# Optimization experiments

Hardware: AMD Instinct MI355X
Metric: run time of the kernel (lower is better)

The kernel has to match this reference:

```python
import jax, jax.numpy as jnp
import numpy as np

REG1 = 0.05
REG2 = 0.05

N, D, P = 262144, 256, 512


def setup_inputs() -> dict:
    key = jax.random.key(0)
    kz, kp = jax.random.split(key)
    z = jax.random.normal(kz, (N, D), dtype=jnp.float32)
    # nn.Parameter(torch.rand(P, D)) -> uniform [0, 1)
    prototype_vectors = jax.random.uniform(kp, (P, D), dtype=jnp.float32)
    return {"z": z, "prototype_vectors": prototype_vectors}


def _cdist(a, b):
    # Euclidean pairwise distances [Na, Nb] via the norm trick (matches torch.cdist p=2).
    a2 = jnp.sum(a * a, axis=-1, keepdims=True)          # [Na, 1]
    b2 = jnp.sum(b * b, axis=-1)[None, :]                # [1, Nb]
    sq = a2 + b2 - 2.0 * (a @ b.T)
    return jnp.sqrt(jnp.maximum(sq, 0.0))


def reference(z, prototype_vectors):
    p_dist = _cdist(z, prototype_vectors)                # [N, P]
    f_dist = _cdist(prototype_vectors, z)                # [P, N]
    return (REG1 * jnp.mean(jnp.min(p_dist, axis=1))
            + REG2 * jnp.mean(jnp.min(f_dist, axis=1)))
```

## Files before the change

kernel.cpp:

```cpp
#include <hip/hip_runtime.h>
#include <hip/hip_bf16.h>

#define N_ROWS 262144
#define DDIM   256
#define PROTO  512
#define BM     64
#define RTG    4096
#define NBLK   8192

typedef __bf16 bf16x8 __attribute__((ext_vector_type(8)));
typedef float  f32x4  __attribute__((ext_vector_type(4)));

__global__ void prep_proto(const float* __restrict__ Pm,
                           unsigned short* __restrict__ PBf,
                           float* __restrict__ P2) {
  int p = blockIdx.x;
  int k = threadIdx.x;
  float v = Pm[p * DDIM + k];
  int idx = (p >> 4) * 4096 + (k >> 5) * 512 + ((((k >> 3) & 3) * 16) + (p & 15)) * 8 + (k & 7);
  ((__bf16*)PBf)[idx] = (__bf16)v;
  float sq = v * v;
  #pragma unroll
  for (int m = 1; m < 64; m <<= 1) sq += __shfl_xor(sq, m);
  __shared__ float ws4[4];
  if ((k & 63) == 0) ws4[k >> 6] = sq;
  __syncthreads();
  if (k == 0) P2[p] = (ws4[0] + ws4[1]) + (ws4[2] + ws4[3]);
}

__global__ __launch_bounds__(256, 4)
void proto_main(const float* __restrict__ Z, const unsigned short* __restrict__ PBf,
                const float* __restrict__ P2, float* __restrict__ colpart,
                float* __restrict__ rowminpart) {
  __shared__ __align__(16) unsigned short A_lds[BM * 256];
  __shared__ float z2s[BM];
  __shared__ float rowred[BM * 4];

  const int t   = threadIdx.x;
  const int w   = t >> 6;
  const int l   = t & 63;
  const int l15 = l & 15;
  const int lg  = l >> 4;

  const int bid = blockIdx.x;
  const int g   = ((bid >> 4) << 3) | (bid & 7);
  const int cc  = (bid >> 3) & 1;
  const size_t row0 = (size_t)g * BM;

  const int srow = t >> 2;
  const int sc4  = t & 3;
  {
    const float4* Zv = (const float4*)Z + (row0 + srow) * (DDIM / 4);
    float zacc = 0.f;
    #pragma unroll
    for (int m = 0; m < 8; ++m) {
      float4 a0 = Zv[(sc4 + m * 4) * 2];
      float4 a1 = Zv[(sc4 + m * 4) * 2 + 1];
      zacc += a0.x*a0.x + a0.y*a0.y + a0.z*a0.z + a0.w*a0.w
            + a1.x*a1.x + a1.y*a1.y + a1.z*a1.z + a1.w*a1.w;
      bf16x8 pk;
      pk[0] = (__bf16)a0.x; pk[1] = (__bf16)a0.y; pk[2] = (__bf16)a0.z; pk[3] = (__bf16)a0.w;
      pk[4] = (__bf16)a1.x; pk[5] = (__bf16)a1.y; pk[6] = (__bf16)a1.z; pk[7] = (__bf16)a1.w;
      int slot = (sc4 + m * 4) ^ (srow & 7);
      *(bf16x8*)&A_lds[srow * 256 + slot * 8] = pk;
    }
    zacc += __shfl_xor(zacc, 1);
    zacc += __shfl_xor(zacc, 2);
    if (sc4 == 0) z2s[srow] = zacc;
  }

  float p2r[4];
  #pragma unroll
  for (int j = 0; j < 4; ++j) p2r[j] = P2[cc * 256 + w * 64 + j * 16 + l15];

  __syncthreads();

  f32x4 acc[4][4];
  #pragma unroll
  for (int i = 0; i < 4; ++i)
    #pragma unroll
    for (int j = 0; j < 4; ++j)
      acc[i][j] = (f32x4){0.f, 0.f, 0.f, 0.f};

  const unsigned short* PBw = PBf + (size_t)(cc * 16 + w * 4) * 4096 + l * 8;
  bf16x8 bgn[4];
  #pragma unroll
  for (int j = 0; j < 4; ++j)
    bgn[j] = *(const bf16x8*)&PBw[(size_t)(j * 8) * 512];
  #pragma unroll
  for (int ks = 0; ks < 8; ++ks) {
    bf16x8 bgc[4];
    #pragma unroll
    for (int j = 0; j < 4; ++j) bgc[j] = bgn[j];
    if (ks < 7) {
      #pragma unroll
      for (int j = 0; j < 4; ++j)
        bgn[j] = *(const bf16x8*)&PBw[(size_t)(j * 8 + ks + 1) * 512];
    }
    __builtin_amdgcn_s_setprio(1);
    #pragma unroll
    for (int i = 0; i < 4; ++i) {
      bf16x8 af = *(const bf16x8*)&A_lds[(i * 16 + l15) * 256 + (((ks * 4 + lg) ^ (l15 & 7)) * 8)];
      #pragma unroll
      for (int j = 0; j < 4; ++j)
        acc[i][j] = __builtin_amdgcn_mfma_f32_16x16x32_bf16(af, bgc[j], acc[i][j], 0, 0, 0);
    }
    __builtin_amdgcn_s_setprio(0);
  }

  float cmin[4] = {3.4e38f, 3.4e38f, 3.4e38f, 3.4e38f};
  #pragma unroll
  for (int i = 0; i < 4; ++i) {
    #pragma unroll
    for (int r = 0; r < 4; ++r) {
      int arow = i * 16 + lg * 4 + r;
      float z2 = z2s[arow];
      float m = 3.4e38f;
      #pragma unroll
      for (int j = 0; j < 4; ++j) {
        float sq = fmaxf(z2 + p2r[j] - 2.0f * acc[i][j][r], 0.0f);
        m = fminf(m, sq);
        cmin[j] = fminf(cmin[j], sq);
      }
      m = fminf(m, __shfl_xor(m, 1));
      m = fminf(m, __shfl_xor(m, 2));
      m = fminf(m, __shfl_xor(m, 4));
      m = fminf(m, __shfl_xor(m, 8));
      if (l15 == 0) rowred[arow * 4 + w] = m;
    }
  }
  #pragma unroll
  for (int j = 0; j < 4; ++j) {
    float c = cmin[j];
    c = fminf(c, __shfl_xor(c, 16));
    c = fminf(c, __shfl_xor(c, 32));
    cmin[j] = c;
  }
  if (l < 16) {
    #pragma unroll
    for (int j = 0; j < 4; ++j)
      colpart[(size_t)g * PROTO + cc * 256 + w * 64 + j * 16 + l] = cmin[j];
  }
  __syncthreads();
  if (t < 64) {
    float m = fminf(fminf(rowred[t * 4], rowred[t * 4 + 1]),
                    fminf(rowred[t * 4 + 2], rowred[t * 4 + 3]));
    rowminpart[(size_t)cc * N_ROWS + row0 + t] = m;
  }
}

__global__ void col_reduce(const float* __restrict__ colpart, float* __restrict__ colfin) {
  int t    = threadIdx.x;
  int colb = blockIdx.x * 16;
  int cl   = t & 15;
  int gg   = t >> 4;
  float m = 3.4e38f;
  for (int g = gg; g < RTG; g += 32)
    m = fminf(m, colpart[(size_t)g * PROTO + colb + cl]);
  m = fminf(m, __shfl_xor(m, 16));
  m = fminf(m, __shfl_xor(m, 32));
  __shared__ float red[8][16];
  if ((t & 63) < 16) red[t >> 6][cl] = m;
  __syncthreads();
  if (t < 16) {
    float r = red[0][t];
    #pragma unroll
    for (int wv = 1; wv < 8; ++wv) r = fminf(r, red[wv][t]);
    colfin[colb + t] = sqrtf(r);
  }
}

__global__ void row_reduce(const float* __restrict__ rowminpart, float* __restrict__ rowsum) {
  int t = threadIdx.x;
  size_t grow = (size_t)blockIdx.x * 256 + t;
  float m = fminf(rowminpart[grow], rowminpart[N_ROWS + grow]);
  float s = sqrtf(m);
  #pragma unroll
  for (int mm = 1; mm < 64; mm <<= 1) s += __shfl_xor(s, mm);
  __shared__ float ws4[4];
  if ((t & 63) == 0) ws4[t >> 6] = s;
  __syncthreads();
  if (t == 0) rowsum[blockIdx.x] = (ws4[0] + ws4[1]) + (ws4[2] + ws4[3]);
}

__global__ void final_reduce(const float* __restrict__ colfin,
                             const float* __restrict__ rowsum,
                             float* __restrict__ out) {
  int t = threadIdx.x;
  float sc = colfin[t];
  float sr = rowsum[t] + rowsum[t + 512];
  #pragma unroll
  for (int mm = 1; mm < 64; mm <<= 1) { sc += __shfl_xor(sc, mm); sr += __shfl_xor(sr, mm); }
  __shared__ float wc[8], wr[8];
  if ((t & 63) == 0) { wc[t >> 6] = sc; wr[t >> 6] = sr; }
  __syncthreads();
  if (t == 0) {
    float tc = 0.f, tr = 0.f;
    #pragma unroll
    for (int i = 0; i < 8; ++i) { tc += wc[i]; tr += wr[i]; }
    out[0] = 0.05f * (tr / (float)N_ROWS) + 0.05f * (tc / (float)PROTO);
  }
}

extern "C" void kernel_launch(void* const* d_in, const int* in_sizes, int n_in,
                              void* d_out, int out_size, void* d_ws, size_t ws_size,
                              hipStream_t stream) {
  const float* z  = (const float*)d_in[0];
  const float* pv = (const float*)d_in[1];
  char* ws = (char*)d_ws;
  size_t off = 0;
  unsigned short* PBf = (unsigned short*)(ws + off); off += 262144;
  float* P2           = (float*)(ws + off);          off += 2048;
  float* colpart      = (float*)(ws + off);          off += (size_t)RTG * PROTO * 4;
  float* colfin       = (float*)(ws + off);          off += 2048;
  float* rowminpart   = (float*)(ws + off);          off += (size_t)2 * N_ROWS * 4;
  float* rowsum       = (float*)(ws + off);          off += 4096;

  prep_proto<<<PROTO, DDIM, 0, stream>>>(pv, PBf, P2);
  proto_main<<<NBLK, 256, 0, stream>>>(z, PBf, P2, colpart, rowminpart);
  col_reduce<<<32, 512, 0, stream>>>(colpart, colfin);
  row_reduce<<<N_ROWS / 256, 256, 0, stream>>>(rowminpart, rowsum);
  final_reduce<<<1, PROTO, 0, stream>>>(colfin, rowsum, (float*)d_out);
}
```

Measured before the change: 141.9 us.

## Stage Z tile as fp32 via direct global-to-LDS loads, convert in main loop

Replaces the register-staged Z load (convert to bf16, compute row norms, write to LDS) with global_load_lds DMA of fp32 data into LDS using a swizzled source layout. The bf16 conversion and the z-squared norm accumulation move into the MFMA loop, with the norms shuffle-reduced afterward. LDS per block doubles to 64KB, so launch bounds drop occupancy from 4 to 2 blocks. The intent is to cut VGPR staging and load latency, at the cost of extra conversion ALU work in the MFMA loop, an added barrier, and lower occupancy.

Result: slower. 292.0 us (+105.7%).

```diff
diff --git a/kernel.cpp b/kernel.cpp
--- a/kernel.cpp
+++ b/kernel.cpp
@@ -28,11 +28,11 @@
   if (k == 0) P2[p] = (ws4[0] + ws4[1]) + (ws4[2] + ws4[3]);
 }
 
-__global__ __launch_bounds__(256, 4)
+__global__ __launch_bounds__(256, 2)
 void proto_main(const float* __restrict__ Z, const unsigned short* __restrict__ PBf,
                 const float* __restrict__ P2, float* __restrict__ colpart,
                 float* __restrict__ rowminpart) {
-  __shared__ __align__(16) unsigned short A_lds[BM * 256];
+  __shared__ __align__(16) float A_lds[BM * 256];
   __shared__ float z2s[BM];
   __shared__ float rowred[BM * 4];
 
@@ -47,31 +47,30 @@
   const int cc  = (bid >> 3) & 1;
   const size_t row0 = (size_t)g * BM;
 
-  const int srow = t >> 2;
-  const int sc4  = t & 3;
   {
-    const float4* Zv = (const float4*)Z + (row0 + srow) * (DDIM / 4);
-    float zacc = 0.f;
-    #pragma unroll
-    for (int m = 0; m < 8; ++m) {
-      float4 a0 = Zv[(sc4 + m * 4) * 2];
-      float4 a1 = Zv[(sc4 + m * 4) * 2 + 1];
-      zacc += a0.x*a0.x + a0.y*a0.y + a0.z*a0.z + a0.w*a0.w
-            + a1.x*a1.x + a1.y*a1.y + a1.z*a1.z + a1.w*a1.w;
-      bf16x8 pk;
-      pk[0] = (__bf16)a0.x; pk[1] = (__bf16)a0.y; pk[2] = (__bf16)a0.z; pk[3] = (__bf16)a0.w;
-      pk[4] = (__bf16)a1.x; pk[5] = (__bf16)a1.y; pk[6] = (__bf16)a1.z; pk[7] = (__bf16)a1.w;
-      int slot = (sc4 + m * 4) ^ (srow & 7);
-      *(bf16x8*)&A_lds[srow * 256 + slot * 8] = pk;
-    }
-    zacc += __shfl_xor(zacc, 1);
-    zacc += __shfl_xor(zacc, 2);
-    if (sc4 == 0) z2s[srow] = zacc;
+    const int half = l & 1;
+    const int slot = l >> 1;
+    #pragma unroll
+    for (int q = 0; q < 16; ++q) {
+      const int rr   = w * 16 + q;
+      const int lcol = ((slot ^ (q & 7)) << 3) + (half << 2);
+      const float* src = Z + (row0 + rr) * DDIM + lcol;
+      __builtin_amdgcn_global_load_lds(
+          (const __attribute__((address_space(1))) void*)src,
+          (__attribute__((address_space(3))) void*)&A_lds[rr * 256],
+          16, 0, 0);
+    }
   }
 
   float p2r[4];
   #pragma unroll
   for (int j = 0; j < 4; ++j) p2r[j] = P2[cc * 256 + w * 64 + j * 16 + l15];
+
+  const unsigned short* PBw = PBf + (size_t)(cc * 16 + w * 4) * 4096 + l * 8;
+  bf16x8 bgn[4];
+  #pragma unroll
+  for (int j = 0; j < 4; ++j)
+    bgn[j] = *(const bf16x8*)&PBw[(size_t)(j * 8) * 512];
 
   __syncthreads();
 
@@ -81,12 +80,8 @@
     #pragma unroll
     for (int j = 0; j < 4; ++j)
       acc[i][j] = (f32x4){0.f, 0.f, 0.f, 0.f};
-
-  const unsigned short* PBw = PBf + (size_t)(cc * 16 + w * 4) * 4096 + l * 8;
-  bf16x8 bgn[4];
-  #pragma unroll
-  for (int j = 0; j < 4; ++j)
-    bgn[j] = *(const bf16x8*)&PBw[(size_t)(j * 8) * 512];
+  float z2p[4] = {0.f, 0.f, 0.f, 0.f};
+
   #pragma unroll
   for (int ks = 0; ks < 8; ++ks) {
     bf16x8 bgc[4];
@@ -100,13 +95,35 @@
     __builtin_amdgcn_s_setprio(1);
     #pragma unroll
     for (int i = 0; i < 4; ++i) {
-      bf16x8 af = *(const bf16x8*)&A_lds[(i * 16 + l15) * 256 + (((ks * 4 + lg) ^ (l15 & 7)) * 8)];
+      const int r = i * 16 + l15;
+      const int s = (ks * 4 + lg) ^ (l15 & 7);
+      const float* base = &A_lds[r * 256 + s * 8];
+      float4 f0 = *(const float4*)base;
+      float4 f1 = *(const float4*)(base + 4);
+      z2p[i] = fmaf(f0.x, f0.x, z2p[i]); z2p[i] = fmaf(f0.y, f0.y, z2p[i]);
+      z2p[i] = fmaf(f0.z, f0.z, z2p[i]); z2p[i] = fmaf(f0.w, f0.w, z2p[i]);
+      z2p[i] = fmaf(f1.x, f1.x, z2p[i]); z2p[i] = fmaf(f1.y, f1.y, z2p[i]);
+      z2p[i] = fmaf(f1.z, f1.z, z2p[i]); z2p[i] = fmaf(f1.w, f1.w, z2p[i]);
+      bf16x8 af;
+      af[0] = (__bf16)f0.x; af[1] = (__bf16)f0.y; af[2] = (__bf16)f0.z; af[3] = (__bf16)f0.w;
+      af[4] = (__bf16)f1.x; af[5] = (__bf16)f1.y; af[6] = (__bf16)f1.z; af[7] = (__bf16)f1.w;
       #pragma unroll
       for (int j = 0; j < 4; ++j)
         acc[i][j] = __builtin_amdgcn_mfma_f32_16x16x32_bf16(af, bgc[j], acc[i][j], 0, 0, 0);
     }
     __builtin_amdgcn_s_setprio(0);
   }
+
+  #pragma unroll
+  for (int i = 0; i < 4; ++i) {
+    z2p[i] += __shfl_xor(z2p[i], 16);
+    z2p[i] += __shfl_xor(z2p[i], 32);
+  }
+  if (w == 0 && l < 16) {
+    #pragma unroll
+    for (int i = 0; i < 4; ++i) z2s[i * 16 + l15] = z2p[i];
+  }
+  __syncthreads();
 
   float cmin[4] = {3.4e38f, 3.4e38f, 3.4e38f, 3.4e38f};
   #pragma unroll
```
